# Kernel optimization log

Hardware: AMD Instinct MI355X
Metric: run time of the kernel (lower is better)

The kernel has to match this reference:

```python
import jax, jax.numpy as jnp
import numpy as np

B, T, C, H = 16, 2048, 1024, 64

def setup_inputs() -> dict:
    key = jax.random.key(0)
    kx, kq, kk, kv = jax.random.split(key, 4)
    x = jax.random.normal(kx, (B, T, C), dtype=jnp.float32)
    Wq = jax.random.normal(kq, (C, H), dtype=jnp.float32) * (C ** -0.5)
    Wk = jax.random.normal(kk, (C, H), dtype=jnp.float32) * (C ** -0.5)
    Wv = jax.random.normal(kv, (C, H), dtype=jnp.float32) * (C ** -0.5)
    return {"x": x, "Wq": Wq, "Wk": Wk, "Wv": Wv}

def reference(x, Wq, Wk, Wv):
    # q,k,v: [B,T,H]
    q = jnp.einsum('btc,ch->bth', x, Wq)
    k = jnp.einsum('btc,ch->bth', x, Wk)
    v = jnp.einsum('btc,ch->bth', x, Wv)
    scale = k.shape[-1] ** -0.5
    # scores: [B,T,T], causal mask then softmax (dropout=0 -> identity)
    w = jnp.einsum('bth,bsh->bts', q, k) * scale
    causal = jnp.tril(jnp.ones((x.shape[1], x.shape[1]), dtype=bool))
    w = jnp.where(causal[None, :, :], w, -jnp.inf)
    w = jax.nn.softmax(w, axis=-1)
    out = jnp.einsum('bts,bsh->bth', w, v)
    return out
```

## Files before the change

### kernel.cpp

```cpp
#include <hip/hip_runtime.h>


#define B_ 16
#define T_ 2048
#define C_ 1024
#define H_ 64
#define QK_ELEMS (B_ * T_ * H_)

typedef float  f32x4  __attribute__((ext_vector_type(4)));
typedef __bf16 bf16x8 __attribute__((ext_vector_type(8)));
typedef __bf16 bf16x4 __attribute__((ext_vector_type(4)));

__device__ __forceinline__ void glds16(const void* g, void* l) {
    __builtin_amdgcn_global_load_lds(
        (const __attribute__((address_space(1))) void*)g,
        (__attribute__((address_space(3))) void*)l, 16, 0, 0);
}

__global__ __launch_bounds__(256) void wt_kernel(const float* __restrict__ Wq,
                                                 const float* __restrict__ Wk,
                                                 const float* __restrict__ Wv,
                                                 __bf16* __restrict__ Wt) {
    __shared__ float tl[64][65];
    const int mat = blockIdx.x >> 4;
    const int c0  = (blockIdx.x & 15) * 64;
    const float* W = (mat == 0) ? Wq : (mat == 1) ? Wk : Wv;
    const int t  = threadIdx.x;
    const int r4 = t >> 6;
    const int cc = t & 63;
#pragma unroll
    for (int i = 0; i < 16; i++) {
        const int c = r4 + i * 4;
        tl[c][cc] = W[(size_t)(c0 + c) * H_ + cc];
    }
    __syncthreads();
#pragma unroll
    for (int i = 0; i < 16; i++) {
        const int h = r4 + i * 4;
        Wt[(size_t)mat * 65536 + (size_t)h * C_ + c0 + cc] = (__bf16)tl[cc][h];
    }
}

__global__ __launch_bounds__(256, 2) void qkv_kernel(const float* __restrict__ x,
                                                     const __bf16* __restrict__ Wt,
                                                     __bf16* __restrict__ Qw,
                                                     __bf16* __restrict__ Kw,
                                                     __bf16* __restrict__ Vtw) {
    __shared__ __align__(16) __bf16 Vt_l[64 * 72];

    const int tid  = threadIdx.x;
    const int w    = tid >> 6;
    const int lane = tid & 63;
    const int quad = lane >> 4;
    const int l15  = lane & 15;
    const int m0   = blockIdx.x * 64;

    f32x4 acc[12];
#pragma unroll
    for (int i = 0; i < 12; i++) acc[i] = (f32x4){0.f, 0.f, 0.f, 0.f};

    const float*  xb = x  + (size_t)(m0 + l15) * C_ + quad * 8;
    const __bf16* wb = Wt + (size_t)(w * 48 + l15) * C_ + quad * 8;

    float4 Aset[3][8];
    bf16x8 Bset[3][3];

    auto loadSet = [&](int h, int s) {
#pragma unroll
        for (int mt = 0; mt < 4; mt++) {
            const float* p = xb + (size_t)mt * 16 * C_ + h * 32;
            Aset[s][mt * 2]     = *(const float4*)p;
            Aset[s][mt * 2 + 1] = *(const float4*)(p + 4);
        }
#pragma unroll
        for (int nt = 0; nt < 3; nt++)
            Bset[s][nt] = *(const bf16x8*)(wb + (size_t)nt * 16 * C_ + h * 32);
    };

    loadSet(0, 0);
    loadSet(1, 1);

#pragma unroll
    for (int h = 0; h < 32; h++) {
        if (h + 2 < 32) loadSet(h + 2, (h + 2) % 3);
        const int s = h % 3;
        bf16x8 af[4];
#pragma unroll
        for (int mt = 0; mt < 4; mt++) {
            const float4 f0 = Aset[s][mt * 2];
            const float4 f1 = Aset[s][mt * 2 + 1];
            af[mt][0] = (__bf16)f0.x; af[mt][1] = (__bf16)f0.y;
            af[mt][2] = (__bf16)f0.z; af[mt][3] = (__bf16)f0.w;
            af[mt][4] = (__bf16)f1.x; af[mt][5] = (__bf16)f1.y;
            af[mt][6] = (__bf16)f1.z; af[mt][7] = (__bf16)f1.w;
        }
#pragma unroll
        for (int mt = 0; mt < 4; mt++)
#pragma unroll
            for (int nt = 0; nt < 3; nt++)
                acc[mt * 3 + nt] = __builtin_amdgcn_mfma_f32_16x16x32_bf16(
                    af[mt], Bset[s][nt], acc[mt * 3 + nt], 0, 0, 0);
    }

#pragma unroll
    for (int mt = 0; mt < 4; mt++) {
        const int row0 = m0 + mt * 16 + quad * 4;
#pragma unroll
        for (int nt = 0; nt < 3; nt++) {
            const int col = w * 48 + nt * 16 + l15;
            const f32x4 a = acc[mt * 3 + nt];
            if (col < 64) {
#pragma unroll
                for (int r = 0; r < 4; r++)
                    Qw[(size_t)(row0 + r) * H_ + col] = (__bf16)a[r];
            } else if (col < 128) {
                const int h = col - 64;
#pragma unroll
                for (int r = 0; r < 4; r++) {
                    const int row = row0 + r;
                    const int hs  = (((h >> 3) ^ (row & 7)) << 3) | (h & 7);
                    Kw[(size_t)row * H_ + hs] = (__bf16)a[r];
                }
            } else {
                const int h  = col - 128;
                const int t0 = mt * 16 + quad * 4;
                bf16x4 pv;
                pv[0] = (__bf16)a[0]; pv[1] = (__bf16)a[1];
                pv[2] = (__bf16)a[2]; pv[3] = (__bf16)a[3];
                *(bf16x4*)&Vt_l[h * 72 + t0] = pv;
            }
        }
    }
    __syncthreads();
    {
        const int bb   = m0 >> 11;
        const int tblk = m0 & 2047;
#pragma unroll
        for (int i = 0; i < 2; i++) {
            const int idx = tid + i * 256;
            const int h   = idx >> 3;
            const int c   = idx & 7;
            const int sc  = c ^ (h & 7);
            *(bf16x8*)(Vtw + (((size_t)(bb * H_ + h)) << 11) + tblk + c * 8) =
                *(const bf16x8*)&Vt_l[h * 72 + sc * 8];
        }
    }
}

#define SCALE_LOG2E 0.18033688011112042f

__global__ __launch_bounds__(256) void attn_kernel(const __bf16* __restrict__ Qw,
                                                   const __bf16* __restrict__ Kw,
                                                   const __bf16* __restrict__ Vtw,
                                                   float* __restrict__ Opart,
                                                   float* __restrict__ Lpart) {
    __shared__ __align__(16) __bf16 Klds[2][64 * 64];
    __shared__ __align__(16) __bf16 Vlds[2][64 * 64];
    __shared__ __align__(16) __bf16 Plds[2][4][16 * 72];

    const int tid  = threadIdx.x;
    const int w    = tid >> 6;
    const int lane = tid & 63;
    const int quad = lane >> 4;
    const int l15  = lane & 15;

    const int b   = blockIdx.x & 15;
    const int cid = blockIdx.x >> 4;
    int i, ci;
    if (cid < 16)      { i = 15 - (cid >> 2); ci = cid & 3; }
    else if (cid < 28) { const int u = cid - 16; i = 11 - u / 3; ci = u % 3; }
    else if (cid < 36) { const int u = cid - 28; i = 7 - (u >> 1); ci = u & 1; }
    else               { i = 3 - (cid - 36); ci = 0; }

    const int jmax = 2 * i + 1;
    const int j0 = ci * 8;
    const int j1 = (j0 + 8 < jmax + 1) ? j0 + 8 : jmax + 1;
    const int nj = j1 - j0;
    const int qA0 = 2 * i * 64;
    const size_t bT = (size_t)b * T_;

    const __bf16* qpA = Qw + (bT + qA0 + w * 16 + l15) * H_ + quad * 8;
    const bf16x8 qfA0 = *(const bf16x8*)qpA;
    const bf16x8 qfA1 = *(const bf16x8*)(qpA + 32);
    const bf16x8 qfB0 = *(const bf16x8*)(qpA + 64 * H_);
    const bf16x8 qfB1 = *(const bf16x8*)(qpA + 64 * H_ + 32);

    float lA = 0.f, lB = 0.f;
    f32x4 accA[4], accB[4];
#pragma unroll
    for (int nt = 0; nt < 4; nt++) {
        accA[nt] = (f32x4){0.f, 0.f, 0.f, 0.f};
        accB[nt] = (f32x4){0.f, 0.f, 0.f, 0.f};
    }

    auto stage = [&](int ts0, int buf) {
        const __bf16* Ks = Kw + (bT + ts0) * H_;
        const __bf16* Vs = Vtw + (((size_t)(b * H_)) << 11) + ts0;
#pragma unroll
        for (int c = 0; c < 2; c++) {
            const int g   = w * 2 + c;
            const int row = g * 8 + (lane >> 3);
            const int cb  = (lane & 7) * 8;
            glds16(Ks + (size_t)row * H_ + cb, &Klds[buf][g * 512]);
            glds16(Vs + ((size_t)row << 11) + cb, &Vlds[buf][g * 512]);
        }
    };

    stage(j0 * 64, 0);

    for (int jj = 0; jj < nj; jj++) {
        const int j = j0 + jj;
        __syncthreads();
        if (jj + 1 < nj) stage((j + 1) * 64, (jj + 1) & 1);
        const int buf = jj & 1;
        const bool doA = (j <= 2 * i);
        const int ts0 = j * 64;
        const int qgA = qA0 + w * 16 + l15;

#pragma unroll
        for (int nt = 0; nt < 4; nt++) {
            const __bf16* kb = &Klds[buf][(nt * 16 + l15) * 64];
            bf16x8 kf0 = *(const bf16x8*)(kb + ((quad ^ (l15 & 7)) << 3));
            bf16x8 kf1 = *(const bf16x8*)(kb + (((4 + quad) ^ (l15 & 7)) << 3));
            const int key0 = ts0 + nt * 16 + quad * 4;

            if (doA) {
                f32x4 z = (f32x4){0.f, 0.f, 0.f, 0.f};
                z = __builtin_amdgcn_mfma_f32_16x16x32_bf16(kf0, qfA0, z, 0, 0, 0);
                z = __builtin_amdgcn_mfma_f32_16x16x32_bf16(kf1, qfA1, z, 0, 0, 0);
                bf16x4 pv;
#pragma unroll
                for (int r = 0; r < 4; r++) {
                    float e = exp2f(__builtin_fmaf(z[r], SCALE_LOG2E, -8.0f));
                    if (j == 2 * i && key0 + r > qgA) e = 0.f;
                    pv[r] = (__bf16)e;
                    lA += e;
                }
                *(bf16x4*)&Plds[0][w][l15 * 72 + nt * 16 + quad * 4] = pv;
            }
            {
                f32x4 z = (f32x4){0.f, 0.f, 0.f, 0.f};
                z = __builtin_amdgcn_mfma_f32_16x16x32_bf16(kf0, qfB0, z, 0, 0, 0);
                z = __builtin_amdgcn_mfma_f32_16x16x32_bf16(kf1, qfB1, z, 0, 0, 0);
                bf16x4 pv;
#pragma unroll
                for (int r = 0; r < 4; r++) {
                    float e = exp2f(__builtin_fmaf(z[r], SCALE_LOG2E, -8.0f));
                    if (j == jmax && key0 + r > qgA + 64) e = 0.f;
                    pv[r] = (__bf16)e;
                    lB += e;
                }
                *(bf16x4*)&Plds[1][w][l15 * 72 + nt * 16 + quad * 4] = pv;
            }
        }
        __asm__ __volatile__("s_waitcnt lgkmcnt(0)" ::: "memory");

        const __bf16* prA = &Plds[0][w][l15 * 72];
        const __bf16* prB = &Plds[1][w][l15 * 72];
        bf16x8 pfA0, pfA1;
        if (doA) {
            pfA0 = *(const bf16x8*)(prA + quad * 8);
            pfA1 = *(const bf16x8*)(prA + 32 + quad * 8);
        }
        bf16x8 pfB0 = *(const bf16x8*)(prB + quad * 8);
        bf16x8 pfB1 = *(const bf16x8*)(prB + 32 + quad * 8);
#pragma unroll
        for (int nt = 0; nt < 4; nt++) {
            const __bf16* vb = &Vlds[buf][(nt * 16 + l15) * 64];
            bf16x8 vf0 = *(const bf16x8*)(vb + ((quad ^ (l15 & 7)) << 3));
            bf16x8 vf1 = *(const bf16x8*)(vb + (((4 + quad) ^ (l15 & 7)) << 3));
            if (doA) {
                accA[nt] = __builtin_amdgcn_mfma_f32_16x16x32_bf16(pfA0, vf0, accA[nt], 0, 0, 0);
                accA[nt] = __builtin_amdgcn_mfma_f32_16x16x32_bf16(pfA1, vf1, accA[nt], 0, 0, 0);
            }
            accB[nt] = __builtin_amdgcn_mfma_f32_16x16x32_bf16(pfB0, vf0, accB[nt], 0, 0, 0);
            accB[nt] = __builtin_amdgcn_mfma_f32_16x16x32_bf16(pfB1, vf1, accB[nt], 0, 0, 0);
        }
    }

    lA += __shfl_xor(lA, 16); lA += __shfl_xor(lA, 32);
    lB += __shfl_xor(lB, 16); lB += __shfl_xor(lB, 32);

    const int qiA = 2 * i;
    const int slotA = ((((b << 5) + qiA) << 2) + ci);
    const int slotB = ((((b << 5) + qiA + 1) << 2) + ci);
    float* OpA = Opart + (size_t)slotA * 4096;
    float* OpB = Opart + (size_t)slotB * 4096;
#pragma unroll
    for (int nt = 0; nt < 4; nt++)
#pragma unroll
        for (int r = 0; r < 4; r++) {
            const int o = (w * 16 + quad * 4 + r) * 64 + nt * 16 + l15;
            OpA[o] = accA[nt][r];
            OpB[o] = accB[nt][r];
        }
    if (quad == 0) {
        Lpart[slotA * 64 + w * 16 + l15] = lA;
        Lpart[slotB * 64 + w * 16 + l15] = lB;
    }
}

__global__ __launch_bounds__(256) void reduce_kernel(const float* __restrict__ Opart,
                                                     const float* __restrict__ Lpart,
                                                     float* __restrict__ out) {
    const int b  = blockIdx.x & 15;
    const int qi = blockIdx.x >> 4;
    const int nc = ((qi & ~1) + 9) >> 3;
    const int tid = threadIdx.x;
    const int q  = tid >> 2;
    const int hc = (tid & 3) * 16;
    const int sbase = ((b << 5) + qi) << 2;

    f32x4 s[4];
#pragma unroll
    for (int i = 0; i < 4; i++) s[i] = (f32x4){0.f, 0.f, 0.f, 0.f};
    float l = 0.f;
    for (int ci = 0; ci < nc; ci++) {
        const float* Op = Opart + (size_t)(sbase + ci) * 4096 + q * 64 + hc;
#pragma unroll
        for (int i = 0; i < 4; i++) s[i] += *(const f32x4*)(Op + i * 4);
        l += Lpart[(sbase + ci) * 64 + q];
    }
    const float inv = 1.f / l;
    float* o = out + ((size_t)b * T_ + qi * 64 + q) * H_ + hc;
#pragma unroll
    for (int i = 0; i < 4; i++) {
        f32x4 r = s[i] * inv;
        *(f32x4*)(o + i * 4) = r;
    }
}

extern "C" void kernel_launch(void* const* d_in, const int* in_sizes, int n_in,
                              void* d_out, int out_size, void* d_ws, size_t ws_size,
                              hipStream_t stream) {
    const float* x  = (const float*)d_in[0];
    const float* Wq = (const float*)d_in[1];
    const float* Wk = (const float*)d_in[2];
    const float* Wv = (const float*)d_in[3];
    float* out = (float*)d_out;

    __bf16* Qw  = (__bf16*)d_ws;
    __bf16* Kw  = Qw + QK_ELEMS;
    __bf16* Vtw = Kw + QK_ELEMS;
    __bf16* Wt  = Vtw + QK_ELEMS;
    float* Opart = (float*)((char*)d_ws + 16777216);
    float* Lpart = Opart + (size_t)2048 * 4096;

    wt_kernel<<<dim3(48), dim3(256), 0, stream>>>(Wq, Wk, Wv, Wt);
    qkv_kernel<<<dim3((B_ * T_) / 64), dim3(256), 0, stream>>>(x, Wt, Qw, Kw, Vtw);
    attn_kernel<<<dim3(640), dim3(256), 0, stream>>>(Qw, Kw, Vtw, Opart, Lpart);
    reduce_kernel<<<dim3(512), dim3(256), 0, stream>>>(Opart, Lpart, out);
}
```

Before: 291.2 us.

## Restructure QKV projection to stage tiles through LDS with async weight loads

The QKV projection kernel now computes 32-row tiles instead of 64, doubling the grid and raising the occupancy hint. Each k-step converts x to bf16 once into double-buffered shared memory, and weight tiles arrive via async global-to-LDS loads with an XOR swizzle, replacing per-wave register prefetching of x and W. The goal is to cut redundant global loads and register pressure so more waves can hide latency. The costs are a barrier per k-step and the fact that W is reread by twice as many blocks.

```diff
diff --git a/kernel.cpp b/kernel.cpp
--- a/kernel.cpp
+++ b/kernel.cpp
@@ -41,69 +41,81 @@
     }
 }
 
-__global__ __launch_bounds__(256, 2) void qkv_kernel(const float* __restrict__ x,
+__global__ __launch_bounds__(256, 4) void qkv_kernel(const float* __restrict__ x,
                                                      const __bf16* __restrict__ Wt,
                                                      __bf16* __restrict__ Qw,
                                                      __bf16* __restrict__ Kw,
                                                      __bf16* __restrict__ Vtw) {
-    __shared__ __align__(16) __bf16 Vt_l[64 * 72];
+    __shared__ __align__(16) __bf16 Alds[2][32 * 40];
+    __shared__ __align__(16) __bf16 Blds[2][192 * 32];
 
     const int tid  = threadIdx.x;
     const int w    = tid >> 6;
     const int lane = tid & 63;
     const int quad = lane >> 4;
     const int l15  = lane & 15;
-    const int m0   = blockIdx.x * 64;
-
-    f32x4 acc[12];
-#pragma unroll
-    for (int i = 0; i < 12; i++) acc[i] = (f32x4){0.f, 0.f, 0.f, 0.f};
-
-    const float*  xb = x  + (size_t)(m0 + l15) * C_ + quad * 8;
-    const __bf16* wb = Wt + (size_t)(w * 48 + l15) * C_ + quad * 8;
-
-    float4 Aset[3][8];
-    bf16x8 Bset[3][3];
-
-    auto loadSet = [&](int h, int s) {
-#pragma unroll
-        for (int mt = 0; mt < 4; mt++) {
-            const float* p = xb + (size_t)mt * 16 * C_ + h * 32;
-            Aset[s][mt * 2]     = *(const float4*)p;
-            Aset[s][mt * 2 + 1] = *(const float4*)(p + 4);
-        }
-#pragma unroll
-        for (int nt = 0; nt < 3; nt++)
-            Bset[s][nt] = *(const bf16x8*)(wb + (size_t)nt * 16 * C_ + h * 32);
+    const int m0   = blockIdx.x * 32;
+
+    f32x4 acc[6];
+#pragma unroll
+    for (int i = 0; i < 6; i++) acc[i] = (f32x4){0.f, 0.f, 0.f, 0.f};
+
+    const int ar = tid >> 3;
+    const int ac = (tid & 7) * 4;
+    const float* xA = x + (size_t)(m0 + ar) * C_ + ac;
+
+    int bsrc_off[3];
+#pragma unroll
+    for (int i = 0; i < 3; i++) {
+        const int P  = i * 256 + w * 64 + lane;
+        const int pr = P >> 3, pc = P & 7;
+        const int s  = pc ^ (pr & 7);
+        const int rl = pr * 2 + (s >> 2);
+        const int c  = s & 3;
+        bsrc_off[i] = rl * C_ + c * 8;
+    }
+
+    float4 a_reg;
+    auto loadA = [&](int k0) { a_reg = *(const float4*)(xA + k0); };
+    auto storeA = [&](int buf) {
+        bf16x4 v;
+        v[0] = (__bf16)a_reg.x; v[1] = (__bf16)a_reg.y;
+        v[2] = (__bf16)a_reg.z; v[3] = (__bf16)a_reg.w;
+        *(bf16x4*)&Alds[buf][ar * 40 + ac] = v;
     };
-
-    loadSet(0, 0);
-    loadSet(1, 1);
-
-#pragma unroll
-    for (int h = 0; h < 32; h++) {
-        if (h + 2 < 32) loadSet(h + 2, (h + 2) % 3);
-        const int s = h % 3;
-        bf16x8 af[4];
-#pragma unroll
-        for (int mt = 0; mt < 4; mt++) {
-            const float4 f0 = Aset[s][mt * 2];
-            const float4 f1 = Aset[s][mt * 2 + 1];
-            af[mt][0] = (__bf16)f0.x; af[mt][1] = (__bf16)f0.y;
-            af[mt][2] = (__bf16)f0.z; af[mt][3] = (__bf16)f0.w;
-            af[mt][4] = (__bf16)f1.x; af[mt][5] = (__bf16)f1.y;
-            af[mt][6] = (__bf16)f1.z; af[mt][7] = (__bf16)f1.w;
-        }
-#pragma unroll
-        for (int mt = 0; mt < 4; mt++)
-#pragma unroll
-            for (int nt = 0; nt < 3; nt++)
-                acc[mt * 3 + nt] = __builtin_amdgcn_mfma_f32_16x16x32_bf16(
-                    af[mt], Bset[s][nt], acc[mt * 3 + nt], 0, 0, 0);
-    }
-
-#pragma unroll
-    for (int mt = 0; mt < 4; mt++) {
+    auto asyncB = [&](int k0, int buf) {
+#pragma unroll
+        for (int i = 0; i < 3; i++)
+            glds16(Wt + bsrc_off[i] + k0, &Blds[buf][(i * 256 + w * 64) * 8]);
+    };
+
+    loadA(0); asyncB(0, 0); storeA(0);
+
+    for (int k = 0; k < 32; k++) {
+        __syncthreads();
+        const int kn = k + 1;
+        if (kn < 32) { asyncB(kn * 32, kn & 1); loadA(kn * 32); }
+        const int buf = k & 1;
+
+        bf16x8 af0 = *(const bf16x8*)&Alds[buf][l15 * 40 + quad * 8];
+        bf16x8 af1 = *(const bf16x8*)&Alds[buf][(16 + l15) * 40 + quad * 8];
+#pragma unroll
+        for (int nt = 0; nt < 3; nt++) {
+            const int r  = w * 48 + nt * 16 + l15;
+            const int pr = r >> 1;
+            const int pc = (quad + ((r & 1) << 2)) ^ (pr & 7);
+            bf16x8 bfr = *(const bf16x8*)&Blds[buf][(pr * 8 + pc) * 8];
+            acc[nt]     = __builtin_amdgcn_mfma_f32_16x16x32_bf16(af0, bfr, acc[nt], 0, 0, 0);
+            acc[3 + nt] = __builtin_amdgcn_mfma_f32_16x16x32_bf16(af1, bfr, acc[3 + nt], 0, 0, 0);
+        }
+        if (kn < 32) storeA(kn & 1);
+    }
+
+    __syncthreads();
+
+    __bf16* VtL = &Alds[0][0];
+#pragma unroll
+    for (int mt = 0; mt < 2; mt++) {
         const int row0 = m0 + mt * 16 + quad * 4;
 #pragma unroll
         for (int nt = 0; nt < 3; nt++) {
@@ -127,7 +139,7 @@
                 bf16x4 pv;
                 pv[0] = (__bf16)a[0]; pv[1] = (__bf16)a[1];
                 pv[2] = (__bf16)a[2]; pv[3] = (__bf16)a[3];
-                *(bf16x4*)&Vt_l[h * 72 + t0] = pv;
+                *(bf16x4*)&VtL[h * 40 + t0] = pv;
             }
         }
     }
@@ -135,15 +147,13 @@
     {
         const int bb   = m0 >> 11;
         const int tblk = m0 & 2047;
-#pragma unroll
-        for (int i = 0; i < 2; i++) {
-            const int idx = tid + i * 256;
-            const int h   = idx >> 3;
-            const int c   = idx & 7;
-            const int sc  = c ^ (h & 7);
-            *(bf16x8*)(Vtw + (((size_t)(bb * H_ + h)) << 11) + tblk + c * 8) =
-                *(const bf16x8*)&Vt_l[h * 72 + sc * 8];
-        }
+        const int Gb   = tblk & ~63;
+        const int g    = (tblk >> 5) & 1;
+        const int h    = tid >> 2;
+        const int c    = tid & 3;
+        const int p    = ((g << 2) + c) ^ (h & 7);
+        *(bf16x8*)(Vtw + (((size_t)(bb * H_ + h)) << 11) + Gb + p * 8) =
+            *(const bf16x8*)&VtL[h * 40 + c * 8];
     }
 }
 
@@ -347,7 +357,7 @@
     float* Lpart = Opart + (size_t)2048 * 4096;
 
     wt_kernel<<<dim3(48), dim3(256), 0, stream>>>(Wq, Wk, Wv, Wt);
-    qkv_kernel<<<dim3((B_ * T_) / 64), dim3(256), 0, stream>>>(x, Wt, Qw, Kw, Vtw);
+    qkv_kernel<<<dim3((B_ * T_) / 32), dim3(256), 0, stream>>>(x, Wt, Qw, Kw, Vtw);
     attn_kernel<<<dim3(640), dim3(256), 0, stream>>>(Qw, Kw, Vtw, Opart, Lpart);
     reduce_kernel<<<dim3(512), dim3(256), 0, stream>>>(Opart, Lpart, out);
 }
```

Result: faster. 267.4 us (-8.2%).
